# Performance work log

Measured on AMD Instinct MI355X. Metric: run time of the kernel, lower is better.

Reference implementation:

```python
import jax, jax.numpy as jnp
import numpy as np
import math

DIM = 1024
HEADS = 16
HEAD_DIM = DIM // HEADS
B, N = 1, 4096


def setup_inputs() -> dict:
    key = jax.random.key(0)
    k1, k2, k3, k4 = jax.random.split(key, 4)
    content = jax.random.normal(k1, (B, N, DIM), dtype=jnp.float32)
    # Original initializes projections as identity; perturb slightly so the
    # projections are non-trivial while staying well-conditioned.
    Wq = jnp.eye(DIM, dtype=jnp.float32) + 0.02 * jax.random.normal(k2, (DIM, DIM), dtype=jnp.float32)
    Wk = jnp.eye(DIM, dtype=jnp.float32) + 0.02 * jax.random.normal(k3, (DIM, DIM), dtype=jnp.float32)
    Wv = jnp.eye(DIM, dtype=jnp.float32) + 0.02 * jax.random.normal(k4, (DIM, DIM), dtype=jnp.float32)
    return {"content": content, "Wq": Wq, "Wk": Wk, "Wv": Wv}


def reference(content, Wq, Wk, Wv):
    b, n, d = content.shape
    # QKV projections: [B,N,D] @ [D,D]
    Q = (content @ Wq).reshape(b, n, HEADS, HEAD_DIM)
    K = (content @ Wk).reshape(b, n, HEADS, HEAD_DIM)
    V = (content @ Wv).reshape(b, n, HEADS, HEAD_DIM)
    # torch.split along the last dim == reshape into [.., HEADS, HEAD_DIM]
    scores = jnp.einsum('bqhd,bkhd->bhqk', Q, K) / math.sqrt(HEAD_DIM)
    alpha = jax.nn.softmax(scores, axis=-1)
    # Faithful to the original: masking zeroes the upper triangle AFTER the
    # softmax (no renormalization). With B=1 this applies to the whole batch,
    # exactly as the original loop (which only touches batch index 0).
    causal = jnp.tril(jnp.ones((n, n), dtype=bool))
    alpha = jnp.where(causal, alpha, jnp.zeros((), dtype=alpha.dtype))
    Y = jnp.einsum('bhqk,bkhd->bqhd', alpha, V).reshape(b, n, d)
    return Y
```

## Files before the change

### kernel.cpp

```cpp
#include <hip/hip_runtime.h>
#include <stdint.h>

#define DIMC 1024
#define NSEQ 4096
#define NH 16
#define QSCALE 0.18033688011112042f

typedef __attribute__((ext_vector_type(8))) short bf16x8;
typedef __attribute__((ext_vector_type(4))) float f32x4;
typedef __attribute__((ext_vector_type(16))) float f32x16;

__device__ __forceinline__ unsigned short f2bf(float x) {
    union { float f; unsigned int u; } v; v.f = x;
    unsigned int u = v.u;
    return (unsigned short)((u + 0x7fffu + ((u >> 16) & 1u)) >> 16);
}

__device__ __forceinline__ unsigned cvt_pk_bf16(float lo, float hi) {
    unsigned r;
    asm("v_cvt_pk_bf16_f32 %0, %1, %2" : "=v"(r) : "v"(lo), "v"(hi));
    return r;
}

__device__ __forceinline__ void gload16(const unsigned short* g, unsigned short* l) {
    __builtin_amdgcn_global_load_lds(
        (const __attribute__((address_space(1))) void*)g,
        (__attribute__((address_space(3))) void*)l, 16, 0, 0);
}

__global__ __launch_bounds__(256) void k_conv(const float* __restrict__ in,
                                              unsigned short* __restrict__ out) {
    int i = (blockIdx.x * 256 + threadIdx.x) * 8;
    float4 a = *reinterpret_cast<const float4*>(in + i);
    float4 b = *reinterpret_cast<const float4*>(in + i + 4);
    union { unsigned short us[8]; uint4 v; } r;
    r.us[0] = f2bf(a.x); r.us[1] = f2bf(a.y); r.us[2] = f2bf(a.z); r.us[3] = f2bf(a.w);
    r.us[4] = f2bf(b.x); r.us[5] = f2bf(b.y); r.us[6] = f2bf(b.z); r.us[7] = f2bf(b.w);
    *reinterpret_cast<uint4*>(out + i) = r.v;
}

__global__ __launch_bounds__(1024) void k_wt(const float* __restrict__ Wq,
                                             const float* __restrict__ Wk,
                                             const float* __restrict__ Wv,
                                             unsigned short* __restrict__ wt) {
    __shared__ float tile[32][33];
    int z = blockIdx.z;
    const float* W = (z == 0) ? Wq : ((z == 1) ? Wk : Wv);
    int n0 = blockIdx.x * 32, k0 = blockIdx.y * 32;
    tile[threadIdx.y][threadIdx.x] = W[(k0 + threadIdx.y) * DIMC + n0 + threadIdx.x];
    __syncthreads();
    wt[(size_t)z * DIMC * DIMC + (n0 + threadIdx.y) * DIMC + k0 + threadIdx.x] =
        f2bf(tile[threadIdx.x][threadIdx.y]);
}

__global__ __launch_bounds__(256) void k_gemm(const unsigned short* __restrict__ A,
                                              const unsigned short* __restrict__ Wt,
                                              unsigned short* __restrict__ Qb,
                                              unsigned short* __restrict__ Kb,
                                              unsigned short* __restrict__ Vt) {
    __shared__ unsigned short As[128 * 32];
    __shared__ unsigned short Bs[128 * 32];
    const int z = blockIdx.z;
    const unsigned short* Wz = Wt + (size_t)z * DIMC * DIMC;
    const int n0 = blockIdx.x * 128, m0 = blockIdx.y * 128;
    const int t = threadIdx.x;
    const int w = t >> 6, l = t & 63;
    const int wr = w >> 1, wc = w & 1;
    const int lq = l & 15, lg = l >> 4;
    const int srow = l >> 2, scol = (l & 3) * 8;
    const unsigned short* gA = A  + (size_t)(m0 + w * 32 + srow) * DIMC + scol;
    const unsigned short* gB = Wz + (size_t)(n0 + w * 32 + srow) * DIMC + scol;
    unsigned short* lA = &As[(2 * w) * 512];
    unsigned short* lB = &Bs[(2 * w) * 512];

    f32x4 acc[4][4];
    #pragma unroll
    for (int i = 0; i < 4; ++i)
        #pragma unroll
        for (int j = 0; j < 4; ++j)
            acc[i][j] = f32x4{0.f, 0.f, 0.f, 0.f};

    for (int k0 = 0; k0 < DIMC; k0 += 32) {
        __syncthreads();
        gload16(gA + k0, lA);
        gload16(gA + k0 + 16 * DIMC, lA + 512);
        gload16(gB + k0, lB);
        gload16(gB + k0 + 16 * DIMC, lB + 512);
        __syncthreads();
        bf16x8 af[4], bfr[4];
        #pragma unroll
        for (int mf = 0; mf < 4; ++mf)
            af[mf] = *reinterpret_cast<const bf16x8*>(&As[(wr * 64 + mf * 16 + lq) * 32 + lg * 8]);
        #pragma unroll
        for (int nf = 0; nf < 4; ++nf)
            bfr[nf] = *reinterpret_cast<const bf16x8*>(&Bs[(wc * 64 + nf * 16 + lq) * 32 + lg * 8]);
        __builtin_amdgcn_s_setprio(1);
        #pragma unroll
        for (int mf = 0; mf < 4; ++mf)
            #pragma unroll
            for (int nf = 0; nf < 4; ++nf)
                acc[mf][nf] = __builtin_amdgcn_mfma_f32_16x16x32_bf16(af[mf], bfr[nf], acc[mf][nf], 0, 0, 0);
        __builtin_amdgcn_s_setprio(0);
    }

    if (z < 2) {
        unsigned short* out = (z == 0) ? Qb : Kb;
        const float osc = (z == 0) ? QSCALE : 1.0f;
        #pragma unroll
        for (int mf = 0; mf < 4; ++mf)
            #pragma unroll
            for (int nf = 0; nf < 4; ++nf)
                #pragma unroll
                for (int j = 0; j < 4; ++j) {
                    int row = m0 + wr * 64 + mf * 16 + lg * 4 + j;
                    int col = n0 + wc * 64 + nf * 16 + lq;
                    out[row * DIMC + col] = f2bf(acc[mf][nf][j] * osc);
                }
    } else {
        #pragma unroll
        for (int mf = 0; mf < 4; ++mf)
            #pragma unroll
            for (int nf = 0; nf < 4; ++nf) {
                int row  = n0 + wc * 64 + nf * 16 + lq;
                int colb = m0 + wr * 64 + mf * 16 + lg * 4;
                uint2 pk;
                pk.x = cvt_pk_bf16(acc[mf][nf][0], acc[mf][nf][1]);
                pk.y = cvt_pk_bf16(acc[mf][nf][2], acc[mf][nf][3]);
                *reinterpret_cast<uint2*>(Vt + (size_t)row * NSEQ + colb) = pk;
            }
    }
}

#define KIDX(r, c) ((r) * 64 + ((c) ^ (((r) & 7) * 8)))

#define PV_STEP(SF, s16, kk) do {                                              \
    unsigned C0a = cvt_pk_bf16(SF[8*(s16)+0], SF[8*(s16)+1]);                  \
    unsigned C0b = cvt_pk_bf16(SF[8*(s16)+2], SF[8*(s16)+3]);                  \
    unsigned C1a = cvt_pk_bf16(SF[8*(s16)+4], SF[8*(s16)+5]);                  \
    unsigned C1b = cvt_pk_bf16(SF[8*(s16)+6], SF[8*(s16)+7]);                  \
    unsigned x0 = (unsigned)__shfl_xor((int)C0a, 32);                          \
    unsigned x2 = (unsigned)__shfl_xor((int)C0b, 32);                          \
    unsigned x1 = (unsigned)__shfl_xor((int)C1a, 32);                          \
    unsigned x3 = (unsigned)__shfl_xor((int)C1b, 32);                          \
    union { uint4 u; bf16x8 b; } pcv;                                          \
    pcv.u.x = hi ? x1 : C0a;                                                   \
    pcv.u.y = hi ? x3 : C0b;                                                   \
    pcv.u.z = hi ? C1a : x0;                                                   \
    pcv.u.w = hi ? C1b : x2;                                                   \
    bf16x8 vb0 = *reinterpret_cast<const bf16x8*>(&Vs[cur][KIDX(q32, (kk)*16 + hi*8)]);      \
    bf16x8 vb1 = *reinterpret_cast<const bf16x8*>(&Vs[cur][KIDX(32 + q32, (kk)*16 + hi*8)]); \
    O0 = __builtin_amdgcn_mfma_f32_32x32x16_bf16(pcv.b, vb0, O0, 0, 0, 0);     \
    O1 = __builtin_amdgcn_mfma_f32_32x32x16_bf16(pcv.b, vb1, O1, 0, 0, 0);     \
} while (0)

__global__ __launch_bounds__(256) void k_attn(const unsigned short* __restrict__ Qb,
                                              const unsigned short* __restrict__ Kb,
                                              const unsigned short* __restrict__ Vt,
                                              float* __restrict__ Y) {
    __shared__ unsigned short Ks[2][64 * 64];
    __shared__ unsigned short Vs[2][64 * 64];
    const int bid = blockIdx.x;
    const int x = bid & 7, i = bid >> 3;
    const int h = x * 2 + (i >> 5);
    const int bx = i & 31;
    const int t = threadIdx.x;
    const int w = t >> 6, l = t & 63;
    const int half = w >> 1, wq = w & 1;
    const int q32 = l & 31, hi = l >> 5;
    const int qbA = bx, qbB = 63 - bx;
    const int qb_my = half ? qbB : qbA;
    const int vmax = qbB, pvmax = qb_my;
    const int qrel = wq * 32 + q32;

    bf16x8 qf[4];
    {
        const unsigned short* qp = Qb + (size_t)(qb_my * 64 + qrel) * DIMC + h * 64 + hi * 8;
        qf[0] = *reinterpret_cast<const bf16x8*>(qp);
        qf[1] = *reinterpret_cast<const bf16x8*>(qp + 16);
        qf[2] = *reinterpret_cast<const bf16x8*>(qp + 32);
        qf[3] = *reinterpret_cast<const bf16x8*>(qp + 48);
    }
    float m_fr = -__builtin_inff(), l_st = 0.f;
    f32x16 O0, O1;
    #pragma unroll
    for (int j = 0; j < 16; ++j) { O0[j] = 0.f; O1[j] = 0.f; }

    const int r0 = t >> 3, c0 = (t & 7) * 8;
    const unsigned short* gK = Kb + (size_t)r0 * DIMC + h * 64 + c0;
    const unsigned short* gV = Vt + (size_t)(h * 64 + r0) * NSEQ + c0;
    const int o_lo = KIDX(r0, c0);
    const int o_hi = o_lo + 32 * 64;

    *reinterpret_cast<uint4*>(&Ks[0][o_lo]) = *reinterpret_cast<const uint4*>(gK);
    *reinterpret_cast<uint4*>(&Ks[0][o_hi]) = *reinterpret_cast<const uint4*>(gK + 32 * DIMC);
    *reinterpret_cast<uint4*>(&Vs[0][o_lo]) = *reinterpret_cast<const uint4*>(gV);
    *reinterpret_cast<uint4*>(&Vs[0][o_hi]) = *reinterpret_cast<const uint4*>(gV + 32 * NSEQ);
    uint4 kv0 = *reinterpret_cast<const uint4*>(gK + 64 * DIMC);
    uint4 kv1 = *reinterpret_cast<const uint4*>(gK + 96 * DIMC);
    uint4 vv0 = *reinterpret_cast<const uint4*>(gV + 64);
    uint4 vv1 = *reinterpret_cast<const uint4*>(gV + 32 * NSEQ + 64);

    for (int kt = 0; kt < 64; ++kt) {
        const int cur = kt & 1, nxt = cur ^ 1;
        __syncthreads();
        if (kt + 1 < 64) {
            *reinterpret_cast<uint4*>(&Ks[nxt][o_lo]) = kv0;
            *reinterpret_cast<uint4*>(&Ks[nxt][o_hi]) = kv1;
            if (kt + 1 <= vmax) {
                *reinterpret_cast<uint4*>(&Vs[nxt][o_lo]) = vv0;
                *reinterpret_cast<uint4*>(&Vs[nxt][o_hi]) = vv1;
            }
        }
        if (kt + 2 < 64) {
            kv0 = *reinterpret_cast<const uint4*>(gK + (size_t)(kt + 2) * 64 * DIMC);
            kv1 = *reinterpret_cast<const uint4*>(gK + (size_t)(kt + 2) * 64 * DIMC + 32 * DIMC);
            if (kt + 2 <= vmax) {
                vv0 = *reinterpret_cast<const uint4*>(gV + (kt + 2) * 64);
                vv1 = *reinterpret_cast<const uint4*>(gV + 32 * NSEQ + (kt + 2) * 64);
            }
        }

        f32x16 s0, s1;
        #pragma unroll
        for (int j = 0; j < 16; ++j) { s0[j] = 0.f; s1[j] = 0.f; }
        __builtin_amdgcn_s_setprio(1);
        #pragma unroll
        for (int c = 0; c < 4; ++c) {
            bf16x8 ka0 = *reinterpret_cast<const bf16x8*>(&Ks[cur][KIDX(q32,      c * 16 + hi * 8)]);
            bf16x8 ka1 = *reinterpret_cast<const bf16x8*>(&Ks[cur][KIDX(32 + q32, c * 16 + hi * 8)]);
            s0 = __builtin_amdgcn_mfma_f32_32x32x16_bf16(ka0, qf[c], s0, 0, 0, 0);
            s1 = __builtin_amdgcn_mfma_f32_32x32x16_bf16(ka1, qf[c], s1, 0, 0, 0);
        }
        __builtin_amdgcn_s_setprio(0);

        float tl = s0[0];
        #pragma unroll
        for (int j = 1; j < 16; ++j) tl = fmaxf(tl, s0[j]);
        #pragma unroll
        for (int j = 0; j < 16; ++j) tl = fmaxf(tl, s1[j]);
        const float tmax = fmaxf(tl, __shfl_xor(tl, 32));

        if (!__all(tmax <= m_fr + 8.f)) {
            const float mnew = fmaxf(m_fr, tmax);
            const float sc = exp2f(m_fr - mnew);
            l_st *= sc;
            #pragma unroll
            for (int j = 0; j < 16; ++j) {
                const float scj = __shfl(sc, (j & 3) + 8 * (j >> 2) + 4 * hi);
                O0[j] *= scj; O1[j] *= scj;
            }
            m_fr = mnew;
        }
        float ps = 0.f;
        #pragma unroll
        for (int j = 0; j < 16; ++j) { const float p = exp2f(s0[j] - m_fr); s0[j] = p; ps += p; }
        #pragma unroll
        for (int j = 0; j < 16; ++j) { const float p = exp2f(s1[j] - m_fr); s1[j] = p; ps += p; }
        ps += __shfl_xor(ps, 32);
        l_st += ps;

        if (kt <= pvmax) {
            if (kt == pvmax) {
                #pragma unroll
                for (int j = 0; j < 16; ++j) {
                    const int kr = (j & 3) + 8 * (j >> 2) + 4 * hi;
                    if (kr > qrel) s0[j] = 0.f;
                    if (32 + kr > qrel) s1[j] = 0.f;
                }
            }
            __builtin_amdgcn_s_setprio(1);
            PV_STEP(s0, 0, 0);
            PV_STEP(s0, 1, 1);
            PV_STEP(s1, 0, 2);
            PV_STEP(s1, 1, 3);
            __builtin_amdgcn_s_setprio(0);
        }
    }

    const float rl = 1.0f / l_st;
    #pragma unroll
    for (int j = 0; j < 16; ++j) {
        const int row = (j & 3) + 8 * (j >> 2) + 4 * hi;
        const float rlj = __shfl(rl, row);
        const size_t yb = (size_t)(qb_my * 64 + wq * 32 + row) * DIMC + h * 64 + q32;
        Y[yb]      = O0[j] * rlj;
        Y[yb + 32] = O1[j] * rlj;
    }
}

extern "C" void kernel_launch(void* const* d_in, const int* in_sizes, int n_in,
                              void* d_out, int out_size, void* d_ws, size_t ws_size,
                              hipStream_t stream) {
    const float* content = (const float*)d_in[0];
    const float* Wq = (const float*)d_in[1];
    const float* Wk = (const float*)d_in[2];
    const float* Wv = (const float*)d_in[3];
    float* Y = (float*)d_out;
    unsigned short* ws  = (unsigned short*)d_ws;
    unsigned short* cbf = ws;
    unsigned short* wt  = cbf + (size_t)NSEQ * DIMC;
    unsigned short* qb  = wt  + (size_t)3 * DIMC * DIMC;
    unsigned short* kb  = qb  + (size_t)NSEQ * DIMC;
    unsigned short* vt  = kb  + (size_t)NSEQ * DIMC;

    hipLaunchKernelGGL(k_conv, dim3(NSEQ * DIMC / (256 * 8)), dim3(256), 0, stream, content, cbf);
    hipLaunchKernelGGL(k_wt,   dim3(32, 32, 3), dim3(32, 32), 0, stream, Wq, Wk, Wv, wt);
    hipLaunchKernelGGL(k_gemm, dim3(DIMC / 128, NSEQ / 128, 3), dim3(256), 0, stream, cbf, wt, qb, kb, vt);
    hipLaunchKernelGGL(k_attn, dim3(512), dim3(256), 0, stream, qb, kb, vt, Y);
}
```

Measured before the change: 261.7 us.

## Split attention key range across two blocks and merge partial softmax results

The attention kernel now splits the key dimension into two halves (split-K / flash-decoding style), launching twice as many blocks, each covering 128 consecutive query rows instead of a paired front/back load-balanced pair. Partial unnormalized outputs and running max/sum are written to workspace, and a new combine kernel rescales and merges them into Y. This aims to raise parallelism and occupancy (launch bounds now request 4 blocks per SM). In exchange it adds an extra kernel launch, partial-output traffic, and loses the previous triangular load balancing.

```diff
diff --git a/kernel.cpp b/kernel.cpp
--- a/kernel.cpp
+++ b/kernel.cpp
@@ -153,28 +153,29 @@
     O1 = __builtin_amdgcn_mfma_f32_32x32x16_bf16(pcv.b, vb1, O1, 0, 0, 0);     \
 } while (0)
 
-__global__ __launch_bounds__(256) void k_attn(const unsigned short* __restrict__ Qb,
-                                              const unsigned short* __restrict__ Kb,
-                                              const unsigned short* __restrict__ Vt,
-                                              float* __restrict__ Y) {
+__global__ __launch_bounds__(256, 4) void k_attn(const unsigned short* __restrict__ Qb,
+                                                 const unsigned short* __restrict__ Kb,
+                                                 const unsigned short* __restrict__ Vt,
+                                                 float* __restrict__ opart,
+                                                 float2* __restrict__ ml) {
     __shared__ unsigned short Ks[2][64 * 64];
     __shared__ unsigned short Vs[2][64 * 64];
     const int bid = blockIdx.x;
-    const int x = bid & 7, i = bid >> 3;
-    const int h = x * 2 + (i >> 5);
-    const int bx = i & 31;
+    const int xcd = bid & 7, i = bid >> 3;
+    const int hc = xcd * 4 + (i >> 5);
+    const int h = hc >> 1, c = hc & 1;
+    const int Q = i & 31;
     const int t = threadIdx.x;
     const int w = t >> 6, l = t & 63;
-    const int half = w >> 1, wq = w & 1;
     const int q32 = l & 31, hi = l >> 5;
-    const int qbA = bx, qbB = 63 - bx;
-    const int qb_my = half ? qbB : qbA;
-    const int vmax = qbB, pvmax = qb_my;
-    const int qrel = wq * 32 + q32;
+    const int diag = 2 * Q + (w >> 1);
+    const int vmax = 2 * Q + 1;
+    const int kt0 = 32 * c, ktN = kt0 + 32;
+    const int qrel = (w & 1) * 32 + q32;
 
     bf16x8 qf[4];
     {
-        const unsigned short* qp = Qb + (size_t)(qb_my * 64 + qrel) * DIMC + h * 64 + hi * 8;
+        const unsigned short* qp = Qb + (size_t)(Q * 128 + w * 32 + q32) * DIMC + h * 64 + hi * 8;
         qf[0] = *reinterpret_cast<const bf16x8*>(qp);
         qf[1] = *reinterpret_cast<const bf16x8*>(qp + 16);
         qf[2] = *reinterpret_cast<const bf16x8*>(qp + 32);
@@ -191,19 +192,24 @@
     const int o_lo = KIDX(r0, c0);
     const int o_hi = o_lo + 32 * 64;
 
-    *reinterpret_cast<uint4*>(&Ks[0][o_lo]) = *reinterpret_cast<const uint4*>(gK);
-    *reinterpret_cast<uint4*>(&Ks[0][o_hi]) = *reinterpret_cast<const uint4*>(gK + 32 * DIMC);
-    *reinterpret_cast<uint4*>(&Vs[0][o_lo]) = *reinterpret_cast<const uint4*>(gV);
-    *reinterpret_cast<uint4*>(&Vs[0][o_hi]) = *reinterpret_cast<const uint4*>(gV + 32 * NSEQ);
-    uint4 kv0 = *reinterpret_cast<const uint4*>(gK + 64 * DIMC);
-    uint4 kv1 = *reinterpret_cast<const uint4*>(gK + 96 * DIMC);
-    uint4 vv0 = *reinterpret_cast<const uint4*>(gV + 64);
-    uint4 vv1 = *reinterpret_cast<const uint4*>(gV + 32 * NSEQ + 64);
-
-    for (int kt = 0; kt < 64; ++kt) {
+    *reinterpret_cast<uint4*>(&Ks[0][o_lo]) = *reinterpret_cast<const uint4*>(gK + (size_t)(kt0 * 64) * DIMC);
+    *reinterpret_cast<uint4*>(&Ks[0][o_hi]) = *reinterpret_cast<const uint4*>(gK + (size_t)(kt0 * 64 + 32) * DIMC);
+    if (kt0 <= vmax) {
+        *reinterpret_cast<uint4*>(&Vs[0][o_lo]) = *reinterpret_cast<const uint4*>(gV + kt0 * 64);
+        *reinterpret_cast<uint4*>(&Vs[0][o_hi]) = *reinterpret_cast<const uint4*>(gV + 32 * NSEQ + kt0 * 64);
+    }
+    uint4 kv0 = *reinterpret_cast<const uint4*>(gK + (size_t)((kt0 + 1) * 64) * DIMC);
+    uint4 kv1 = *reinterpret_cast<const uint4*>(gK + (size_t)((kt0 + 1) * 64 + 32) * DIMC);
+    uint4 vv0, vv1;
+    if (kt0 + 1 <= vmax) {
+        vv0 = *reinterpret_cast<const uint4*>(gV + (kt0 + 1) * 64);
+        vv1 = *reinterpret_cast<const uint4*>(gV + 32 * NSEQ + (kt0 + 1) * 64);
+    }
+
+    for (int kt = kt0; kt < ktN; ++kt) {
         const int cur = kt & 1, nxt = cur ^ 1;
         __syncthreads();
-        if (kt + 1 < 64) {
+        if (kt + 1 < ktN) {
             *reinterpret_cast<uint4*>(&Ks[nxt][o_lo]) = kv0;
             *reinterpret_cast<uint4*>(&Ks[nxt][o_hi]) = kv1;
             if (kt + 1 <= vmax) {
@@ -211,9 +217,9 @@
                 *reinterpret_cast<uint4*>(&Vs[nxt][o_hi]) = vv1;
             }
         }
-        if (kt + 2 < 64) {
-            kv0 = *reinterpret_cast<const uint4*>(gK + (size_t)(kt + 2) * 64 * DIMC);
-            kv1 = *reinterpret_cast<const uint4*>(gK + (size_t)(kt + 2) * 64 * DIMC + 32 * DIMC);
+        if (kt + 2 < ktN) {
+            kv0 = *reinterpret_cast<const uint4*>(gK + (size_t)((kt + 2) * 64) * DIMC);
+            kv1 = *reinterpret_cast<const uint4*>(gK + (size_t)((kt + 2) * 64 + 32) * DIMC);
             if (kt + 2 <= vmax) {
                 vv0 = *reinterpret_cast<const uint4*>(gV + (kt + 2) * 64);
                 vv1 = *reinterpret_cast<const uint4*>(gV + 32 * NSEQ + (kt + 2) * 64);
@@ -225,11 +231,11 @@
         for (int j = 0; j < 16; ++j) { s0[j] = 0.f; s1[j] = 0.f; }
         __builtin_amdgcn_s_setprio(1);
         #pragma unroll
-        for (int c = 0; c < 4; ++c) {
-            bf16x8 ka0 = *reinterpret_cast<const bf16x8*>(&Ks[cur][KIDX(q32,      c * 16 + hi * 8)]);
-            bf16x8 ka1 = *reinterpret_cast<const bf16x8*>(&Ks[cur][KIDX(32 + q32, c * 16 + hi * 8)]);
-            s0 = __builtin_amdgcn_mfma_f32_32x32x16_bf16(ka0, qf[c], s0, 0, 0, 0);
-            s1 = __builtin_amdgcn_mfma_f32_32x32x16_bf16(ka1, qf[c], s1, 0, 0, 0);
+        for (int cc = 0; cc < 4; ++cc) {
+            bf16x8 ka0 = *reinterpret_cast<const bf16x8*>(&Ks[cur][KIDX(q32,      cc * 16 + hi * 8)]);
+            bf16x8 ka1 = *reinterpret_cast<const bf16x8*>(&Ks[cur][KIDX(32 + q32, cc * 16 + hi * 8)]);
+            s0 = __builtin_amdgcn_mfma_f32_32x32x16_bf16(ka0, qf[cc], s0, 0, 0, 0);
+            s1 = __builtin_amdgcn_mfma_f32_32x32x16_bf16(ka1, qf[cc], s1, 0, 0, 0);
         }
         __builtin_amdgcn_s_setprio(0);
 
@@ -259,8 +265,8 @@
         ps += __shfl_xor(ps, 32);
         l_st += ps;
 
-        if (kt <= pvmax) {
-            if (kt == pvmax) {
+        if (kt <= diag) {
+            if (kt == diag) {
                 #pragma unroll
                 for (int j = 0; j < 16; ++j) {
                     const int kr = (j & 3) + 8 * (j >> 2) + 4 * hi;
@@ -277,14 +283,43 @@
         }
     }
 
-    const float rl = 1.0f / l_st;
+    float* op = opart + ((size_t)(c * 16 + h) * 4096 + (size_t)Q * 128 + w * 32) * 64;
     #pragma unroll
     for (int j = 0; j < 16; ++j) {
         const int row = (j & 3) + 8 * (j >> 2) + 4 * hi;
-        const float rlj = __shfl(rl, row);
-        const size_t yb = (size_t)(qb_my * 64 + wq * 32 + row) * DIMC + h * 64 + q32;
-        Y[yb]      = O0[j] * rlj;
-        Y[yb + 32] = O1[j] * rlj;
+        op[row * 64 + q32]      = O0[j];
+        op[row * 64 + 32 + q32] = O1[j];
+    }
+    if (hi == 0)
+        ml[(c * 16 + h) * 4096 + Q * 128 + w * 32 + q32] = make_float2(m_fr, l_st);
+}
+
+__global__ __launch_bounds__(256) void k_comb(const float* __restrict__ opart,
+                                              const float2* __restrict__ ml,
+                                              float* __restrict__ Y) {
+    const int bid = blockIdx.x;
+    const int h = bid >> 6, qb64 = bid & 63;
+    const int t = threadIdx.x;
+    const int r = t >> 2, d0 = (t & 3) * 16;
+    const int q = qb64 * 64 + r;
+    const float2 a = ml[(0 * 16 + h) * 4096 + q];
+    const float2 b = ml[(1 * 16 + h) * 4096 + q];
+    const float M = fmaxf(a.x, b.x);
+    const float w0 = exp2f(a.x - M), w1 = exp2f(b.x - M);
+    const float rL = 1.0f / (a.y * w0 + b.y * w1);
+    const float* o0 = opart + ((size_t)(0 * 16 + h) * 4096 + q) * 64 + d0;
+    const float* o1 = opart + ((size_t)(1 * 16 + h) * 4096 + q) * 64 + d0;
+    float* y = Y + (size_t)q * DIMC + h * 64 + d0;
+    #pragma unroll
+    for (int k = 0; k < 4; ++k) {
+        float4 v0 = *reinterpret_cast<const float4*>(o0 + k * 4);
+        float4 v1 = *reinterpret_cast<const float4*>(o1 + k * 4);
+        float4 o;
+        o.x = (v0.x * w0 + v1.x * w1) * rL;
+        o.y = (v0.y * w0 + v1.y * w1) * rL;
+        o.z = (v0.z * w0 + v1.z * w1) * rL;
+        o.w = (v0.w * w0 + v1.w * w1) * rL;
+        *reinterpret_cast<float4*>(y + k * 4) = o;
     }
 }
 
@@ -302,9 +337,12 @@
     unsigned short* qb  = wt  + (size_t)3 * DIMC * DIMC;
     unsigned short* kb  = qb  + (size_t)NSEQ * DIMC;
     unsigned short* vt  = kb  + (size_t)NSEQ * DIMC;
+    float* opart = (float*)(vt + (size_t)NSEQ * DIMC);
+    float2* mlb  = (float2*)(opart + (size_t)2 * 16 * 4096 * 64);
 
     hipLaunchKernelGGL(k_conv, dim3(NSEQ * DIMC / (256 * 8)), dim3(256), 0, stream, content, cbf);
     hipLaunchKernelGGL(k_wt,   dim3(32, 32, 3), dim3(32, 32), 0, stream, Wq, Wk, Wv, wt);
     hipLaunchKernelGGL(k_gemm, dim3(DIMC / 128, NSEQ / 128, 3), dim3(256), 0, stream, cbf, wt, qb, kb, vt);
-    hipLaunchKernelGGL(k_attn, dim3(512), dim3(256), 0, stream, qb, kb, vt, Y);
-}
+    hipLaunchKernelGGL(k_attn, dim3(1024), dim3(256), 0, stream, qb, kb, vt, opart, mlb);
+    hipLaunchKernelGGL(k_comb, dim3(1024), dim3(256), 0, stream, opart, mlb, Y);
+}
```

New measurement: 273.6 us. +4.5%, slower.
